# Kernel tuning notes

Measured on AMD Instinct MI355X. Metric: run time of the kernel, lower is better.

## Reference

```python
import jax, jax.numpy as jnp
import numpy as np

B, S, D, V, T, NS, NG = 16, 512, 400, 32000, 8, 30, 3


def setup_inputs() -> dict:
    key = jax.random.key(0)
    ks = jax.random.split(key, 14)
    w = 1.0 / np.sqrt(D)
    return {
        "encoded_hidden": jax.random.normal(ks[0], (1, B, D), jnp.float32) * 0.1,
        "encoded_outputs": jax.random.normal(ks[1], (B, S, D), jnp.float32) * 0.1,
        "story": jax.random.randint(ks[2], (B, S), 0, V),
        "trg_batches": jax.random.randint(ks[3], (B, NS, T), 0, V),
        "shared_emb": jax.random.normal(ks[4], (V, D), jnp.float32) * 0.1,
        "slot_emb": jax.random.normal(ks[5], (1, D), jnp.float32) * 0.1,
        "w_ih": jax.random.normal(ks[6], (3 * D, D), jnp.float32) * w,
        "w_hh": jax.random.normal(ks[7], (3 * D, D), jnp.float32) * w,
        "b_ih": jax.random.normal(ks[8], (3 * D,), jnp.float32) * w,
        "b_hh": jax.random.normal(ks[9], (3 * D,), jnp.float32) * w,
        "w_ratio_w": jax.random.normal(ks[10], (1, 3 * D), jnp.float32) * w,
        "w_ratio_b": jax.random.normal(ks[11], (1,), jnp.float32) * w,
        "w_gate_w": jax.random.normal(ks[12], (NG, D), jnp.float32) * w,
        "w_gate_b": jax.random.normal(ks[13], (NG,), jnp.float32) * w,
        "batch_size": B,
        "max_resp_len": T,
    }


def reference(encoded_hidden, encoded_outputs, story, trg_batches, shared_emb,
              slot_emb, w_ih, w_hh, b_ih, b_hh, w_ratio_w, w_ratio_b,
              w_gate_w, w_gate_b, batch_size, max_resp_len):
    # Original torch code returns inside the slot loop -> only slot 0 is decoded.
    # h0 is re-used as GRU initial state at EVERY step (no carried hidden), and
    # teacher forcing makes each step's input known, so all T steps vectorize.
    h0 = encoded_hidden[0]                         # (B, D)
    Bq, Tq = batch_size, max_resp_len
    Vq = shared_emb.shape[0]

    # decoder inputs: step 0 = slot embedding, steps 1..T-1 = emb(trg[:,0,i-1])
    x0 = jnp.broadcast_to(slot_emb, h0.shape)      # (B, D)
    xt = shared_emb[trg_batches[:, 0, : Tq - 1]]   # (B, T-1, D)
    X = jnp.concatenate([x0[:, None, :], xt], axis=1)  # (B, T, D)

    # GRU cell (torch gate order r, z, n), h0 broadcast over steps
    gi = X @ w_ih.T + b_ih                         # (B, T, 3D)
    gh = h0 @ w_hh.T + b_hh                        # (B, 3D)
    i_r, i_z, i_n = jnp.split(gi, 3, axis=-1)
    h_r, h_z, h_n = jnp.split(gh, 3, axis=-1)
    r = jax.nn.sigmoid(i_r + h_r[:, None, :])
    z = jax.nn.sigmoid(i_z + h_z[:, None, :])
    n = jnp.tanh(i_n + r * h_n[:, None, :])
    h = (1.0 - z) * n + z * h0[:, None, :]         # (B, T, D) decoder_state == hidden

    # attention over history (no length masking: all lens == S)
    scores = jnp.einsum('btd,bsd->bts', h, encoded_outputs)   # (B, T, S)
    probs = jax.nn.softmax(scores, axis=-1)
    # FAITHFUL to original bug: context uses raw scores, not probs
    context = jnp.einsum('bts,bsd->btd', scores, encoded_outputs)

    gate0 = context[:, 0, :] @ w_gate_w.T + w_gate_b          # (B, NG), step i==0

    p_vocab = jax.nn.softmax(h @ shared_emb.T, axis=-1)       # (B, T, V)
    p_gen = jax.nn.sigmoid(
        jnp.concatenate([h, context, X], axis=-1) @ w_ratio_w.T + w_ratio_b
    )                                                         # (B, T, 1)

    # pointer distribution: scatter_add probs onto vocab ids of the story
    p_ctx = jnp.zeros((Bq, Tq, Vq), p_vocab.dtype).at[
        jnp.arange(Bq)[:, None, None],
        jnp.arange(Tq)[None, :, None],
        story[:, None, :],
    ].add(probs)

    p_final = p_gen * p_vocab + (1.0 - p_gen) * p_ctx         # (B, T, V)

    ptr_outputs = jnp.zeros((NS, Bq, Tq, Vq), p_final.dtype).at[0].set(p_final)
    gate_outputs = jnp.zeros((NS, Bq, NG), gate0.dtype).at[0].set(gate0)
    return ptr_outputs, gate_outputs
```

## Files before the change

### kernel.cpp

```cpp
#include <hip/hip_runtime.h>

#define Bq 16
#define Sq 512
#define Dq 400
#define Vq 32000
#define Tq 8
#define NSq 30
#define NGq 3
#define BTq (Bq*Tq)
#define D3q (3*Dq)
#define SLICE 4096000
#define PTR_TOTAL (30ull*SLICE)
#define GATE_TOTAL (NSq*Bq*NGq)

__device__ inline float sigmoidf_(float x) { return 1.0f / (1.0f + __expf(-x)); }

__device__ inline float blockReduceSum(float v, float* red) {
    int tid = threadIdx.x;
    #pragma unroll
    for (int o = 32; o > 0; o >>= 1) v += __shfl_down(v, o, 64);
    if ((tid & 63) == 0) red[tid >> 6] = v;
    __syncthreads();
    if (tid == 0) {
        float s = red[0];
        int nw = blockDim.x >> 6;
        for (int i = 1; i < nw; i++) s += red[i];
        red[0] = s;
    }
    __syncthreads();
    float r = red[0];
    __syncthreads();
    return r;
}

__device__ inline float blockReduceMax(float v, float* red) {
    int tid = threadIdx.x;
    #pragma unroll
    for (int o = 32; o > 0; o >>= 1) v = fmaxf(v, __shfl_down(v, o, 64));
    if ((tid & 63) == 0) red[tid >> 6] = v;
    __syncthreads();
    if (tid == 0) {
        float s = red[0];
        int nw = blockDim.x >> 6;
        for (int i = 1; i < nw; i++) s = fmaxf(s, red[i]);
        red[0] = s;
    }
    __syncthreads();
    float r = red[0];
    __syncthreads();
    return r;
}

__global__ void k_prep(const float* __restrict__ enc_hidden, const float* __restrict__ shared_emb,
                       const float* __restrict__ slot_emb, const float* __restrict__ w_ih,
                       const float* __restrict__ w_hh, const float* __restrict__ b_ih,
                       const float* __restrict__ b_hh, const int* __restrict__ trg,
                       float* __restrict__ h_out, float* __restrict__ hT_out,
                       float* __restrict__ X_out) {
    __shared__ float x_l[Dq], h0_l[Dq], gi_l[D3q], gh_l[D3q];
    int bt = blockIdx.x, b = bt >> 3, t = bt & 7;
    int tid = threadIdx.x;
    int tok = (t == 0) ? 0 : trg[b * NSq * Tq + (t - 1)];
    for (int d = tid; d < Dq; d += blockDim.x) {
        x_l[d] = (t == 0) ? slot_emb[d] : shared_emb[(size_t)tok * Dq + d];
        h0_l[d] = enc_hidden[b * Dq + d];
    }
    __syncthreads();
    for (int j = tid; j < D3q; j += blockDim.x) {
        const float4* wi4 = (const float4*)(w_ih + (size_t)j * Dq);
        const float4* wh4 = (const float4*)(w_hh + (size_t)j * Dq);
        float ai = b_ih[j], ah = b_hh[j];
        for (int q = 0; q < Dq / 4; ++q) {
            float4 pi = wi4[q], ph = wh4[q];
            int k = 4 * q;
            ai += x_l[k]*pi.x + x_l[k+1]*pi.y + x_l[k+2]*pi.z + x_l[k+3]*pi.w;
            ah += h0_l[k]*ph.x + h0_l[k+1]*ph.y + h0_l[k+2]*ph.z + h0_l[k+3]*ph.w;
        }
        gi_l[j] = ai; gh_l[j] = ah;
    }
    __syncthreads();
    for (int d = tid; d < Dq; d += blockDim.x) {
        float r = sigmoidf_(gi_l[d] + gh_l[d]);
        float z = sigmoidf_(gi_l[Dq + d] + gh_l[Dq + d]);
        float n = tanhf(gi_l[2 * Dq + d] + r * gh_l[2 * Dq + d]);
        float h = (1.0f - z) * n + z * h0_l[d];
        h_out[bt * Dq + d] = h;
        hT_out[d * BTq + bt] = h;
        X_out[bt * Dq + d] = x_l[d];
    }
}

__global__ void k_attn(const float* __restrict__ hbuf, const float* __restrict__ Xbuf,
                       const float* __restrict__ enc_out, const float* __restrict__ w_ratio_w,
                       const float* __restrict__ w_ratio_b, const float* __restrict__ w_gate_w,
                       const float* __restrict__ w_gate_b,
                       float* __restrict__ probs, float* __restrict__ pgen,
                       float* __restrict__ out_gate) {
    __shared__ float h_l[Dq], ctx_l[Dq], sc_l[Sq], red[8];
    int bt = blockIdx.x, b = bt >> 3, t = bt & 7;
    int tid = threadIdx.x;
    for (int d = tid; d < Dq; d += 512) h_l[d] = hbuf[bt * Dq + d];
    __syncthreads();
    {
        const float4* e4 = (const float4*)(enc_out + ((size_t)(b * Sq + tid)) * Dq);
        float acc = 0.0f;
        for (int q = 0; q < Dq / 4; ++q) {
            float4 p = e4[q];
            int k = 4 * q;
            acc += h_l[k]*p.x + h_l[k+1]*p.y + h_l[k+2]*p.z + h_l[k+3]*p.w;
        }
        sc_l[tid] = acc;
    }
    __syncthreads();
    float myv = sc_l[tid];
    float m = blockReduceMax(myv, red);
    float e = __expf(myv - m);
    float ssum = blockReduceSum(e, red);
    probs[bt * Sq + tid] = e / ssum;
    for (int d = tid; d < Dq; d += 512) {
        float acc = 0.0f;
        for (int s = 0; s < Sq; ++s)
            acc += sc_l[s] * enc_out[((size_t)(b * Sq + s)) * Dq + d];
        ctx_l[d] = acc;
    }
    __syncthreads();
    {
        float part = 0.0f;
        for (int i = tid; i < D3q; i += 512) {
            float v = (i < Dq) ? h_l[i] : (i < 2 * Dq ? ctx_l[i - Dq] : Xbuf[bt * Dq + (i - 2 * Dq)]);
            part += v * w_ratio_w[i];
        }
        float tot = blockReduceSum(part, red);
        if (tid == 0) pgen[bt] = sigmoidf_(tot + w_ratio_b[0]);
    }
    if (t == 0) {
        for (int g = 0; g < NGq; ++g) {
            float part = 0.0f;
            for (int d = tid; d < Dq; d += 512) part += ctx_l[d] * w_gate_w[g * Dq + d];
            float tot = blockReduceSum(part, red);
            if (tid == 0) out_gate[b * NGq + g] = tot + w_gate_b[g];
        }
    }
}

__global__ void k_scatter(const int* __restrict__ story, const float* __restrict__ probs,
                          float* __restrict__ pctx) {
    int bt = blockIdx.x, b = bt >> 3, s = threadIdx.x;
    int tok = story[b * Sq + s];
    atomicAdd(&pctx[(size_t)bt * Vq + tok], probs[bt * Sq + s]);
}

#define TVL 128
#define CKL 40
__global__ __launch_bounds__(256) void k_logits(const float* __restrict__ hT,
                                                const float* __restrict__ emb,
                                                float* __restrict__ logits) {
    __shared__ float eT[CKL][132];
    __shared__ float hL[CKL][132];
    int tid = threadIdx.x;
    int v0 = blockIdx.x * TVL;
    int tx = tid & 15, ty = tid >> 4;
    float acc[8][8];
    #pragma unroll
    for (int j = 0; j < 8; ++j)
        #pragma unroll
        for (int i = 0; i < 8; ++i) acc[j][i] = 0.0f;

    for (int c = 0; c < Dq / CKL; ++c) {
        int k0 = c * CKL;
        const float4* hg = (const float4*)(hT + (size_t)k0 * BTq);
        #pragma unroll
        for (int r = 0; r < 5; ++r) {
            int idx = tid + 256 * r;
            int k = idx >> 5, c4 = idx & 31;
            float4 vd = hg[idx];
            *(float4*)&hL[k][4 * c4] = vd;
        }
        #pragma unroll
        for (int r = 0; r < 5; ++r) {
            int idx = tid + 256 * r;
            int v = idx / 10, q = idx - 10 * v;
            float4 vd = *(const float4*)(emb + (size_t)(v0 + v) * Dq + k0 + 4 * q);
            eT[4*q+0][v] = vd.x; eT[4*q+1][v] = vd.y; eT[4*q+2][v] = vd.z; eT[4*q+3][v] = vd.w;
        }
        __syncthreads();
        #pragma unroll 4
        for (int k = 0; k < CKL; ++k) {
            float4 h0 = *(const float4*)&hL[k][8 * ty];
            float4 h1 = *(const float4*)&hL[k][8 * ty + 4];
            float4 e0 = *(const float4*)&eT[k][8 * tx];
            float4 e1 = *(const float4*)&eT[k][8 * tx + 4];
            float hv[8] = {h0.x, h0.y, h0.z, h0.w, h1.x, h1.y, h1.z, h1.w};
            float ev[8] = {e0.x, e0.y, e0.z, e0.w, e1.x, e1.y, e1.z, e1.w};
            #pragma unroll
            for (int j = 0; j < 8; ++j)
                #pragma unroll
                for (int i = 0; i < 8; ++i)
                    acc[j][i] += hv[j] * ev[i];
        }
        __syncthreads();
    }
    #pragma unroll
    for (int j = 0; j < 8; ++j) {
        int bt = 8 * ty + j;
        float* dst = logits + (size_t)bt * Vq + v0 + 8 * tx;
        *(float4*)dst       = make_float4(acc[j][0], acc[j][1], acc[j][2], acc[j][3]);
        *(float4*)(dst + 4) = make_float4(acc[j][4], acc[j][5], acc[j][6], acc[j][7]);
    }
}

__global__ void k_stats(const float* __restrict__ logits, float* __restrict__ rmax,
                        float* __restrict__ rinv) {
    __shared__ float red[8];
    int row = blockIdx.x, tid = threadIdx.x;
    const float* lr = logits + (size_t)row * Vq;
    float m = -1e30f;
    for (int v = tid; v < Vq; v += 256) m = fmaxf(m, lr[v]);
    m = blockReduceMax(m, red);
    float s = 0.0f;
    for (int v = tid; v < Vq; v += 256) s += __expf(lr[v] - m);
    s = blockReduceSum(s, red);
    if (tid == 0) { rmax[row] = m; rinv[row] = 1.0f / s; }
}

__global__ void k_combine(const float* __restrict__ logits, const float* __restrict__ pctx,
                          const float* __restrict__ rmax, const float* __restrict__ rinv,
                          const float* __restrict__ pgen, float* __restrict__ out) {
    int bt = blockIdx.y;
    int v = blockIdx.x * 256 + threadIdx.x;
    float m = rmax[bt], inv = rinv[bt], pg = pgen[bt];
    size_t idx = (size_t)bt * Vq + v;
    float pv = __expf(logits[idx] - m) * inv;
    out[idx] = pg * pv + (1.0f - pg) * pctx[idx];
}

extern "C" void kernel_launch(void* const* d_in, const int* in_sizes, int n_in,
                              void* d_out, int out_size, void* d_ws, size_t ws_size,
                              hipStream_t stream) {
    const float* enc_hidden = (const float*)d_in[0];
    const float* enc_out    = (const float*)d_in[1];
    const int*   story      = (const int*)d_in[2];
    const int*   trg        = (const int*)d_in[3];
    const float* shared_emb = (const float*)d_in[4];
    const float* slot_emb   = (const float*)d_in[5];
    const float* w_ih       = (const float*)d_in[6];
    const float* w_hh       = (const float*)d_in[7];
    const float* b_ih       = (const float*)d_in[8];
    const float* b_hh       = (const float*)d_in[9];
    const float* w_ratio_w  = (const float*)d_in[10];
    const float* w_ratio_b  = (const float*)d_in[11];
    const float* w_gate_w   = (const float*)d_in[12];
    const float* w_gate_b   = (const float*)d_in[13];

    float* out = (float*)d_out;

    float* logits_buf = out + (size_t)SLICE;
    float* pctx_buf   = out + 2 * (size_t)SLICE;
    float* h_buf      = out + 3 * (size_t)SLICE;
    float* X_buf      = h_buf + 51200;
    float* probs_buf  = X_buf + 51200;
    float* pgen_buf   = probs_buf + 65536;
    float* rmax_buf   = pgen_buf + 128;
    float* rinv_buf   = rmax_buf + 128;
    float* hT_buf     = rinv_buf + 128;

    hipMemsetAsync(pctx_buf, 0, (size_t)SLICE * sizeof(float), stream);

    hipLaunchKernelGGL(k_prep, dim3(BTq), dim3(256), 0, stream,
                       enc_hidden, shared_emb, slot_emb, w_ih, w_hh, b_ih, b_hh, trg,
                       h_buf, hT_buf, X_buf);
    hipLaunchKernelGGL(k_attn, dim3(BTq), dim3(512), 0, stream,
                       h_buf, X_buf, enc_out, w_ratio_w, w_ratio_b, w_gate_w, w_gate_b,
                       probs_buf, pgen_buf, out + PTR_TOTAL);
    hipLaunchKernelGGL(k_scatter, dim3(BTq), dim3(Sq), 0, stream, story, probs_buf, pctx_buf);
    hipLaunchKernelGGL(k_logits, dim3(Vq / TVL), dim3(256), 0, stream,
                       hT_buf, shared_emb, logits_buf);
    hipLaunchKernelGGL(k_stats, dim3(BTq), dim3(256), 0, stream, logits_buf, rmax_buf, rinv_buf);
    hipLaunchKernelGGL(k_combine, dim3(Vq / 256, BTq), dim3(256), 0, stream,
                       logits_buf, pctx_buf, rmax_buf, rinv_buf, pgen_buf, out);

    hipMemsetAsync(out + (size_t)SLICE, 0, (PTR_TOTAL - SLICE) * sizeof(float), stream);
    hipMemsetAsync(out + PTR_TOTAL + Bq * NGq, 0,
                   (size_t)(GATE_TOTAL - Bq * NGq) * sizeof(float), stream);
}
```

Before: 850.8 us.

## Fuse output zero-fill into logits kernel and move scratch buffers to workspace

Moves the logits, pctx and hidden scratch buffers out of the output tensor and into a separate workspace. This lets the large zero-fill of slots 1..29 run inside extra blocks of the logits GEMM kernel, replacing the trailing memsets, so the bandwidth-bound zeroing overlaps with compute. It also unrolls the context reduction loop. The risk is that the zero blocks compete with the GEMM blocks for CUs and memory bandwidth, and the change depends on the workspace being large enough.

Measured after the change: 804.1 us. -5.5%, faster.

```diff
diff --git a/kernel.cpp b/kernel.cpp
--- a/kernel.cpp
+++ b/kernel.cpp
@@ -13,6 +13,10 @@
 #define PTR_TOTAL (30ull*SLICE)
 #define GATE_TOTAL (NSq*Bq*NGq)
 
+#define NCOMPUTE 250
+#define NZERO 1813
+#define ZPER 16384
+
 __device__ inline float sigmoidf_(float x) { return 1.0f / (1.0f + __expf(-x)); }
 
 __device__ inline float blockReduceSum(float v, float* red) {
@@ -119,6 +123,7 @@
     probs[bt * Sq + tid] = e / ssum;
     for (int d = tid; d < Dq; d += 512) {
         float acc = 0.0f;
+        #pragma unroll 8
         for (int s = 0; s < Sq; ++s)
             acc += sc_l[s] * enc_out[((size_t)(b * Sq + s)) * Dq + d];
         ctx_l[d] = acc;
@@ -154,11 +159,31 @@
 #define CKL 40
 __global__ __launch_bounds__(256) void k_logits(const float* __restrict__ hT,
                                                 const float* __restrict__ emb,
-                                                float* __restrict__ logits) {
+                                                float* __restrict__ logits,
+                                                float* __restrict__ out) {
     __shared__ float eT[CKL][132];
     __shared__ float hL[CKL][132];
-    int tid = threadIdx.x;
-    int v0 = blockIdx.x * TVL;
+    int bid = blockIdx.x;
+    int tid = threadIdx.x;
+    if (bid >= NCOMPUTE) {
+        int zb = bid - NCOMPUTE;
+        float4 z = make_float4(0.0f, 0.0f, 0.0f, 0.0f);
+        if (zb < NZERO) {
+            float4* dst = (float4*)(out + (size_t)SLICE);
+            const size_t total = 29ull * SLICE / 4;
+            size_t base = (size_t)zb * ZPER + tid;
+            #pragma unroll
+            for (int r = 0; r < ZPER / 256; ++r) {
+                size_t idx = base + (size_t)r * 256;
+                if (idx < total) dst[idx] = z;
+            }
+        } else {
+            float4* g = (float4*)(out + PTR_TOTAL + Bq * NGq);
+            for (int i = tid; i < (GATE_TOTAL - Bq * NGq) / 4; i += 256) g[i] = z;
+        }
+        return;
+    }
+    int v0 = bid * TVL;
     int tx = tid & 15, ty = tid >> 4;
     float acc[8][8];
     #pragma unroll
@@ -254,9 +279,10 @@
 
     float* out = (float*)d_out;
 
-    float* logits_buf = out + (size_t)SLICE;
-    float* pctx_buf   = out + 2 * (size_t)SLICE;
-    float* h_buf      = out + 3 * (size_t)SLICE;
+    float* ws = (float*)d_ws;
+    float* logits_buf = ws;
+    float* pctx_buf   = ws + (size_t)SLICE;
+    float* h_buf      = ws + 2 * (size_t)SLICE;
     float* X_buf      = h_buf + 51200;
     float* probs_buf  = X_buf + 51200;
     float* pgen_buf   = probs_buf + 65536;
@@ -273,13 +299,9 @@
                        h_buf, X_buf, enc_out, w_ratio_w, w_ratio_b, w_gate_w, w_gate_b,
                        probs_buf, pgen_buf, out + PTR_TOTAL);
     hipLaunchKernelGGL(k_scatter, dim3(BTq), dim3(Sq), 0, stream, story, probs_buf, pctx_buf);
-    hipLaunchKernelGGL(k_logits, dim3(Vq / TVL), dim3(256), 0, stream,
-                       hT_buf, shared_emb, logits_buf);
+    hipLaunchKernelGGL(k_logits, dim3(NCOMPUTE + NZERO + 1), dim3(256), 0, stream,
+                       hT_buf, shared_emb, logits_buf, out);
     hipLaunchKernelGGL(k_stats, dim3(BTq), dim3(256), 0, stream, logits_buf, rmax_buf, rinv_buf);
     hipLaunchKernelGGL(k_combine, dim3(Vq / 256, BTq), dim3(256), 0, stream,
                        logits_buf, pctx_buf, rmax_buf, rinv_buf, pgen_buf, out);
-
-    hipMemsetAsync(out + (size_t)SLICE, 0, (PTR_TOTAL - SLICE) * sizeof(float), stream);
-    hipMemsetAsync(out + PTR_TOTAL + Bq * NGq, 0,
-                   (size_t)(GATE_TOTAL - Bq * NGq) * sizeof(float), stream);
-}
+}
```
